# Optimization experiments

Measured on AMD Instinct MI355X. Metric: run time of the kernel, lower is better.

## Reference

```python
import jax, jax.numpy as jnp
import numpy as np

B, S, H, E, I = 2, 1024, 1024, 8, 512
EPS = 1e-8  # torch F.cosine_similarity eps


def setup_inputs() -> dict:
    key = jax.random.key(0)
    ks = jax.random.split(key, 5)
    return {
        "hidden_states": jax.random.normal(ks[0], (B, S, H), dtype=jnp.float32),
        "expert_embeddings": jax.random.normal(ks[1], (E, H), dtype=jnp.float32),
        # torch init is zeros; -0.03 keeps the zero-selection fallback (which NaNs the
        # original's softmax) from ever triggering while preserving ~half-dense routing
        "gate_threshold": jnp.full((E,), -0.03, dtype=jnp.float32),
        "w_gate": jax.random.normal(ks[2], (E, H, I), dtype=jnp.float32) / np.sqrt(H).astype(np.float32),
        "w_up": jax.random.normal(ks[3], (E, H, I), dtype=jnp.float32) / np.sqrt(H).astype(np.float32),
        "w_down": jax.random.normal(ks[4], (E, I, H), dtype=jnp.float32) / np.sqrt(I).astype(np.float32),
    }


def _forward(hidden_states, expert_embeddings, gate_threshold, w_gate, w_up, w_down):
    b, s, h = hidden_states.shape
    n_experts = expert_embeddings.shape[0]
    x = hidden_states.reshape(-1, h)  # [T, H]

    # cosine-similarity routing scores [T, E]
    xn = x / jnp.maximum(jnp.linalg.norm(x, axis=-1, keepdims=True), EPS)
    en = expert_embeddings / jnp.maximum(jnp.linalg.norm(expert_embeddings, axis=-1, keepdims=True), EPS)
    scores = xn @ en.T

    # SiLUHardThreshold forward: hard 0/1 mask (used only as a boolean downstream,
    # so no gradient flows through it in the module's output path)
    routing_mask = (jax.nn.silu(scores - gate_threshold) > 0).astype(scores.dtype)

    # guarantee at least one expert per token: fall back to top-1 score
    num_sel = routing_mask.sum(axis=-1)  # [T]
    top1 = jnp.argmax(scores, axis=-1)   # [T]
    routing_mask_final = jnp.where((num_sel == 0)[:, None],
                                   jax.nn.one_hot(top1, n_experts, dtype=scores.dtype),
                                   routing_mask)

    # softmax over selected experts (pre-fallback mask, as in the original)
    masked_scores = jnp.where(routing_mask > 0, scores, -jnp.inf)
    routing_weights = jax.nn.softmax(masked_scores.astype(jnp.float32), axis=-1).astype(x.dtype)
    gates = routing_weights * routing_mask_final  # [T, E] combine weights

    # per-expert Qwen3 SwiGLU MLP: down(silu(gate(x)) * up(x)); dense over experts,
    # gated combine is the vectorized equivalent of the gather/MLP/index_add loop
    hmid = jax.nn.silu(jnp.einsum('th,ehi->eti', x, w_gate)) * jnp.einsum('th,ehi->eti', x, w_up)  # [E,T,I]
    out = jnp.einsum('eti,eih,te->th', hmid, w_down, gates)  # [T, H]

    return out.reshape(b, s, h), scores


def reference(hidden_states, expert_embeddings, gate_threshold, w_gate, w_up, w_down):
    # returns (final_hidden_states [B,S,H], router_logits [T,E])
    return _forward(hidden_states, expert_embeddings, gate_threshold, w_gate, w_up, w_down)
```

## Files before the change

### kernel.cpp

```cpp
#include <hip/hip_runtime.h>
#include <hip/hip_bf16.h>
#include <stdint.h>

#define T_TOK 2048
#define H_DIM 1024
#define E_NUM 8
#define I_DIM 512
#define KDOWN (E_NUM * I_DIM)
#define EPSR 1e-8f

typedef short s16x8 __attribute__((ext_vector_type(8)));
typedef float f32x4 __attribute__((ext_vector_type(4)));

static __device__ __forceinline__ uint16_t f2bf(float f) {
    union { float f; uint32_t i; } v; v.f = f;
    uint32_t lsb = (v.i >> 16) & 1u;
    v.i += 0x7fffu + lsb;
    return (uint16_t)(v.i >> 16);
}

static __device__ __forceinline__ void gll16(const void* g, void* l) {
    __builtin_amdgcn_global_load_lds(
        (const __attribute__((address_space(1))) void*)g,
        (__attribute__((address_space(3))) void*)l, 16, 0, 0);
}

__global__ __launch_bounds__(256) void prep_kernel(
    const float* __restrict__ wg, const float* __restrict__ wu,
    const float* __restrict__ wd, uint16_t* __restrict__ wB,
    uint16_t* __restrict__ wdT,
    const float* __restrict__ x, const float* __restrict__ emb,
    const float* __restrict__ thr, float* __restrict__ scores_out,
    float* __restrict__ gates, uint16_t* __restrict__ xb) {
    __shared__ union {
        float tile[64][68];
        struct { float semb[E_NUM * H_DIM]; float senorm[E_NUM]; } r;
    } sm;
    const int bid = blockIdx.x;
    const int tid = threadIdx.x;

    if (bid < 3072) {
        const int bz = bid >> 7, by = (bid >> 3) & 15, bx = bid & 7;
        const int g16 = tid >> 4, l16 = (tid & 15) * 4;
        if (bz < 16) {
            const int e = bz & 7;
            const int isU = (bz >= 8);
            const float* src = (isU ? wu : wg) + (long)e * H_DIM * I_DIM;
            const int r0 = by * 64, c0 = bx * 64;
            #pragma unroll
            for (int it = 0; it < 4; ++it) {
                int r = it * 16 + g16;
                *(float4*)&sm.tile[r][l16] = *(const float4*)(src + (long)(r0 + r) * I_DIM + c0 + l16);
            }
            __syncthreads();
            #pragma unroll
            for (int it = 0; it < 4; ++it) {
                int oc = it * 16 + g16;
                int i = c0 + oc;
                ushort4 o;
                o.x = f2bf(sm.tile[l16 + 0][oc]);
                o.y = f2bf(sm.tile[l16 + 1][oc]);
                o.z = f2bf(sm.tile[l16 + 2][oc]);
                o.w = f2bf(sm.tile[l16 + 3][oc]);
                long rbig = ((long)e << 10) + ((i >> 4) << 5) + (isU << 4) + (i & 15);
                *(ushort4*)(wB + rbig * H_DIM + r0 + l16) = o;
            }
        } else {
            const int e = bz - 16;
            const float* src = wd + (long)e * I_DIM * H_DIM;
            uint16_t* dst = wdT + (long)e * I_DIM;
            const int r0 = bx * 64, c0 = by * 64;
            #pragma unroll
            for (int it = 0; it < 4; ++it) {
                int r = it * 16 + g16;
                *(float4*)&sm.tile[r][l16] = *(const float4*)(src + (long)(r0 + r) * H_DIM + c0 + l16);
            }
            __syncthreads();
            #pragma unroll
            for (int it = 0; it < 4; ++it) {
                int oc = it * 16 + g16;
                ushort4 o;
                o.x = f2bf(sm.tile[l16 + 0][oc]);
                o.y = f2bf(sm.tile[l16 + 1][oc]);
                o.z = f2bf(sm.tile[l16 + 2][oc]);
                o.w = f2bf(sm.tile[l16 + 3][oc]);
                *(ushort4*)(dst + (long)(c0 + oc) * KDOWN + r0 + l16) = o;
            }
        }
        return;
    }
    const int rb = bid - 3072;
    const int lane = tid & 63;
    const int wave = tid >> 6;
    for (int i = tid; i < E_NUM * H_DIM; i += 256) sm.r.semb[i] = emb[i];
    __syncthreads();
    for (int e = wave; e < E_NUM; e += 4) {
        float s = 0.f;
        #pragma unroll
        for (int c = 0; c < 16; ++c) { float v = sm.r.semb[e * H_DIM + lane + 64 * c]; s += v * v; }
        #pragma unroll
        for (int off = 32; off; off >>= 1) s += __shfl_xor(s, off);
        if (lane == 0) sm.r.senorm[e] = fmaxf(sqrtf(s), EPSR);
    }
    __syncthreads();
    const int t = rb * 4 + wave;
    const float* xt = x + (long)t * H_DIM;
    uint16_t* xbt = xb + (long)t * H_DIM;
    float nrm = 0.f, dot[E_NUM];
    #pragma unroll
    for (int e = 0; e < E_NUM; ++e) dot[e] = 0.f;
    #pragma unroll
    for (int c = 0; c < 16; ++c) {
        float v = xt[lane + 64 * c];
        xbt[lane + 64 * c] = f2bf(v);
        nrm += v * v;
        #pragma unroll
        for (int e = 0; e < E_NUM; ++e) dot[e] += v * sm.r.semb[e * H_DIM + lane + 64 * c];
    }
    #pragma unroll
    for (int off = 32; off; off >>= 1) {
        nrm += __shfl_xor(nrm, off);
        #pragma unroll
        for (int e = 0; e < E_NUM; ++e) dot[e] += __shfl_xor(dot[e], off);
    }
    float xn = fmaxf(sqrtf(nrm), EPSR);
    float sc[E_NUM], sel[E_NUM];
    float msel = -1e30f, mall = -1e30f;
    int nsel = 0, arg = 0;
    #pragma unroll
    for (int e = 0; e < E_NUM; ++e) {
        sc[e] = dot[e] / (xn * sm.r.senorm[e]);
        float d = sc[e] - thr[e];
        sel[e] = (d > 0.f) ? 1.f : 0.f;
        if (d > 0.f) { nsel++; msel = fmaxf(msel, sc[e]); }
        if (sc[e] > mall) { mall = sc[e]; arg = e; }
    }
    float w[E_NUM], den = 0.f;
    #pragma unroll
    for (int e = 0; e < E_NUM; ++e) { w[e] = (sel[e] > 0.f) ? __expf(sc[e] - msel) : 0.f; den += w[e]; }
    if (lane == 0) {
        #pragma unroll
        for (int e = 0; e < E_NUM; ++e) {
            scores_out[t * E_NUM + e] = sc[e];
            gates[t * E_NUM + e] = (nsel > 0) ? (w[e] / den) : ((e == arg) ? 1.f : 0.f);
        }
    }
}

__global__ __launch_bounds__(512, 2) void moe_gateup_kernel(
    const uint16_t* __restrict__ xb,
    const uint16_t* __restrict__ wB,
    const float* __restrict__ gates,
    uint16_t* __restrict__ hmid) {
    const int bid = blockIdx.x;
    const int xcd = bid & 7, j = bid >> 3;
    const int by = xcd * 4 + (j >> 3);
    const int bx = j & 7;
    const int t0 = bx * 256;
    const int n0 = by * 256;
    const int e  = by >> 2;

    __shared__ uint16_t sA[4][256][32];
    __shared__ uint16_t sB[4][256][32];
    __shared__ float sGate[256];

    const int tid  = threadIdx.x;
    const int lane = tid & 63;
    const int wave = tid >> 6;
    const int wm = wave >> 2, wn = wave & 3;

    if (tid < 256) sGate[tid] = gates[(t0 + tid) * E_NUM + e];
    __syncthreads();

    const int lr = lane >> 2;
    const int cl = ((lane & 3) ^ ((lane >> 3) & 3)) * 8;
    const uint16_t* gA = xb + (long)(t0 + wave * 16 + lr) * H_DIM + cl;
    const uint16_t* gB = wB + (long)(n0 + wave * 16 + lr) * H_DIM + cl;

#define STA(sl, kt) do { \
        gll16(gA + (long)(kt) * 32,                &sA[sl][wave * 16][0]); \
        gll16(gA + 128L * H_DIM + (long)(kt) * 32, &sA[sl][128 + wave * 16][0]); } while (0)
#define STB(sl, kt) do { \
        gll16(gB + (long)(kt) * 32,                &sB[sl][wave * 16][0]); \
        gll16(gB + 128L * H_DIM + (long)(kt) * 32, &sB[sl][128 + wave * 16][0]); } while (0)

    const int q = lane >> 4, r16 = lane & 15;
    const int pc = (q ^ ((r16 >> 1) & 3)) * 8;

    f32x4 acc[8][4] = {};

    STA(0, 0); STB(0, 0);
    STA(1, 1); STB(1, 1);
    STA(2, 2); STB(2, 2);

    #pragma unroll 1
    for (int s = 0; s < 32; ++s) {
        const int sl = s & 3;
        if (s < 30)       asm volatile("s_waitcnt vmcnt(8)" ::: "memory");
        else if (s == 30) asm volatile("s_waitcnt vmcnt(4)" ::: "memory");
        else              asm volatile("s_waitcnt vmcnt(0)" ::: "memory");
        __builtin_amdgcn_s_barrier();
        asm volatile("" ::: "memory");
        if (s + 3 < 32) { STA((s + 3) & 3, s + 3); STB((s + 3) & 3, s + 3); }
        s16x8 af[8], bf[4];
        #pragma unroll
        for (int m = 0; m < 8; ++m)
            af[m] = *(const s16x8*)&sA[sl][wm * 128 + m * 16 + r16][pc];
        #pragma unroll
        for (int n = 0; n < 4; ++n)
            bf[n] = *(const s16x8*)&sB[sl][wn * 64 + n * 16 + r16][pc];
        __builtin_amdgcn_s_setprio(1);
        #pragma unroll
        for (int m = 0; m < 8; ++m)
            #pragma unroll
            for (int n = 0; n < 4; ++n)
                acc[m][n] = __builtin_amdgcn_mfma_f32_16x16x32_bf16(af[m], bf[n], acc[m][n], 0, 0, 0);
        __builtin_amdgcn_s_setprio(0);
    }
#undef STA
#undef STB

    #pragma unroll
    for (int m = 0; m < 8; ++m) {
        #pragma unroll
        for (int rr = 0; rr < 4; ++rr) {
            const int trow = wm * 128 + m * 16 + q * 4 + rr;
            const float gate = sGate[trow];
            const long tglob = t0 + trow;
            #pragma unroll
            for (int p = 0; p < 2; ++p) {
                float g = acc[m][2 * p][rr], u = acc[m][2 * p + 1][rr];
                float h = gate * (g / (1.f + __expf(-g))) * u;
                const int cb = n0 + wn * 64 + p * 32;
                const int i = (((cb & 1023) >> 5) << 4) + r16;
                hmid[tglob * KDOWN + e * I_DIM + i] = f2bf(h);
            }
        }
    }
}

__global__ __launch_bounds__(256, 2) void moe_down_kernel(
    const uint16_t* __restrict__ hmid,
    const uint16_t* __restrict__ wdT,
    float* __restrict__ out,
    float* __restrict__ parts) {
    const int bid = blockIdx.x + 8 * (blockIdx.y + 16 * blockIdx.z);
    const int r  = bid & 7;
    const int j  = bid >> 3;
    const int h0 = ((r & 1) * 4 + (j & 3)) * 128;
    const int t0 = ((r >> 1) * 4 + ((j >> 2) & 3)) * 128;
    const int kz = j >> 4;
    const int kst = kz * 1024;
    __shared__ uint16_t sA[4][128][32];
    __shared__ uint16_t sB[4][128][32];
    const int tid  = threadIdx.x;
    const int lane = tid & 63;
    const int wave = tid >> 6;
    const int wm = wave >> 1, wn = wave & 1;

    const int lr = lane >> 2;
    const int cl = ((lane & 3) ^ ((lane >> 3) & 3)) * 8;
    const uint16_t* gA = hmid + (long)(t0 + wave * 32 + lr) * KDOWN + kst + cl;
    const uint16_t* gB = wdT  + (long)(h0 + wave * 32 + lr) * KDOWN + kst + cl;

#define STA(sl, kt) do { \
        gll16(gA + (long)(kt) * 32,               &sA[sl][wave * 32][0]); \
        gll16(gA + 16L * KDOWN + (long)(kt) * 32, &sA[sl][wave * 32 + 16][0]); } while (0)
#define STB(sl, kt) do { \
        gll16(gB + (long)(kt) * 32,               &sB[sl][wave * 32][0]); \
        gll16(gB + 16L * KDOWN + (long)(kt) * 32, &sB[sl][wave * 32 + 16][0]); } while (0)

    f32x4 acc[4][4] = {};
    const int q = lane >> 4, r16 = lane & 15;
    const int pc = (q ^ ((r16 >> 1) & 3)) * 8;

    STA(0, 0); STB(0, 0);
    STA(1, 1); STB(1, 1);
    STA(2, 2); STB(2, 2);

    #pragma unroll 1
    for (int s = 0; s < 32; ++s) {
        const int sl = s & 3;
        if (s < 30)       asm volatile("s_waitcnt vmcnt(8)" ::: "memory");
        else if (s == 30) asm volatile("s_waitcnt vmcnt(4)" ::: "memory");
        else              asm volatile("s_waitcnt vmcnt(0)" ::: "memory");
        __builtin_amdgcn_s_barrier();
        asm volatile("" ::: "memory");
        if (s + 3 < 32) { STA((s + 3) & 3, s + 3); STB((s + 3) & 3, s + 3); }
        s16x8 af[4], bf[4];
        #pragma unroll
        for (int m = 0; m < 4; ++m)
            af[m] = *(const s16x8*)&sA[sl][wm * 64 + m * 16 + r16][pc];
        #pragma unroll
        for (int n = 0; n < 4; ++n)
            bf[n] = *(const s16x8*)&sB[sl][wn * 64 + n * 16 + r16][pc];
        __builtin_amdgcn_s_setprio(1);
        #pragma unroll
        for (int m = 0; m < 4; ++m)
            #pragma unroll
            for (int n = 0; n < 4; ++n)
                acc[m][n] = __builtin_amdgcn_mfma_f32_16x16x32_bf16(af[m], bf[n], acc[m][n], 0, 0, 0);
        __builtin_amdgcn_s_setprio(0);
    }
#undef STA
#undef STB

    float* dst = (kz == 0) ? out : (parts + (long)(kz - 1) * T_TOK * H_DIM);
    #pragma unroll
    for (int m = 0; m < 4; ++m) {
        #pragma unroll
        for (int rr = 0; rr < 4; ++rr) {
            const int t = t0 + wm * 64 + m * 16 + q * 4 + rr;
            #pragma unroll
            for (int n = 0; n < 4; ++n)
                dst[(long)t * H_DIM + h0 + wn * 64 + n * 16 + r16] = acc[m][n][rr];
        }
    }
}

__global__ __launch_bounds__(256) void reduce_kernel(float* __restrict__ out,
                                                     const float* __restrict__ parts) {
    long i = ((long)blockIdx.x * 256 + threadIdx.x) * 4;
    float4 a = *(const float4*)(out + i);
    #pragma unroll
    for (int j = 0; j < 3; ++j) {
        float4 b = *(const float4*)(parts + (long)j * T_TOK * H_DIM + i);
        a.x += b.x; a.y += b.y; a.z += b.z; a.w += b.w;
    }
    *(float4*)(out + i) = a;
}

extern "C" void kernel_launch(void* const* d_in, const int* in_sizes, int n_in,
                              void* d_out, int out_size, void* d_ws, size_t ws_size,
                              hipStream_t stream) {
    const float* x    = (const float*)d_in[0];
    const float* emb  = (const float*)d_in[1];
    const float* thr  = (const float*)d_in[2];
    const float* wg   = (const float*)d_in[3];
    const float* wu   = (const float*)d_in[4];
    const float* wd   = (const float*)d_in[5];
    float* out    = (float*)d_out;
    float* scores = out + (size_t)T_TOK * H_DIM;

    uint8_t* ws = (uint8_t*)d_ws;
    uint16_t* xb   = (uint16_t*)(ws);
    uint16_t* wB   = (uint16_t*)(ws + (size_t)4  * 1048576);
    uint16_t* wdT  = (uint16_t*)(ws + (size_t)20 * 1048576);
    uint16_t* hmid = (uint16_t*)(ws + (size_t)28 * 1048576);
    float*    gates = (float*)  (ws + (size_t)44 * 1048576);
    float*    parts = (float*)  (ws + (size_t)48 * 1048576);

    prep_kernel<<<3072 + T_TOK / 4, 256, 0, stream>>>(
        wg, wu, wd, wB, wdT, x, emb, thr, scores, gates, xb);
    moe_gateup_kernel<<<256, 512, 0, stream>>>(xb, wB, gates, hmid);
    moe_down_kernel<<<dim3(H_DIM / 128, T_TOK / 128, 4), 256, 0, stream>>>(hmid, wdT, out, parts);
    reduce_kernel<<<(T_TOK * H_DIM) / 1024, 256, 0, stream>>>(out, parts);
}
```

Before: 187.6 us.

## Split GEMM main loops into two ping-pong phases interleaving loads and MFMA

Both GEMM main loops now run each k-step in two halves. Each half loads part of the B fragments, issues one of the A or B global-to-LDS prefetches, and runs half of the MFMAs, with extra barriers placed between the halves. The aim is to interleave memory issue with matrix work across waves and spread out LDS and global traffic. The cost is four barriers per iteration instead of one, and the vmcnt bookkeeping now has to match the new issue order.

```diff
diff --git a/kernel.cpp b/kernel.cpp
--- a/kernel.cpp
+++ b/kernel.cpp
@@ -192,30 +192,51 @@
     STA(0, 0); STB(0, 0);
     STA(1, 1); STB(1, 1);
     STA(2, 2); STB(2, 2);
+    asm volatile("s_waitcnt vmcnt(8)" ::: "memory");
+    __builtin_amdgcn_s_barrier();
+    asm volatile("" ::: "memory");
 
     #pragma unroll 1
     for (int s = 0; s < 32; ++s) {
         const int sl = s & 3;
-        if (s < 30)       asm volatile("s_waitcnt vmcnt(8)" ::: "memory");
-        else if (s == 30) asm volatile("s_waitcnt vmcnt(4)" ::: "memory");
-        else              asm volatile("s_waitcnt vmcnt(0)" ::: "memory");
-        __builtin_amdgcn_s_barrier();
-        asm volatile("" ::: "memory");
-        if (s + 3 < 32) { STA((s + 3) & 3, s + 3); STB((s + 3) & 3, s + 3); }
         s16x8 af[8], bf[4];
         #pragma unroll
         for (int m = 0; m < 8; ++m)
             af[m] = *(const s16x8*)&sA[sl][wm * 128 + m * 16 + r16][pc];
-        #pragma unroll
-        for (int n = 0; n < 4; ++n)
-            bf[n] = *(const s16x8*)&sB[sl][wn * 64 + n * 16 + r16][pc];
+        bf[0] = *(const s16x8*)&sB[sl][wn * 64 + 0 * 16 + r16][pc];
+        bf[1] = *(const s16x8*)&sB[sl][wn * 64 + 1 * 16 + r16][pc];
+        if (s + 3 < 32) STA((s + 3) & 3, s + 3);
+        asm volatile("" ::: "memory");
+        __builtin_amdgcn_s_barrier();
+        asm volatile("" ::: "memory");
         __builtin_amdgcn_s_setprio(1);
         #pragma unroll
-        for (int m = 0; m < 8; ++m)
-            #pragma unroll
-            for (int n = 0; n < 4; ++n)
-                acc[m][n] = __builtin_amdgcn_mfma_f32_16x16x32_bf16(af[m], bf[n], acc[m][n], 0, 0, 0);
+        for (int m = 0; m < 8; ++m) {
+            acc[m][0] = __builtin_amdgcn_mfma_f32_16x16x32_bf16(af[m], bf[0], acc[m][0], 0, 0, 0);
+            acc[m][1] = __builtin_amdgcn_mfma_f32_16x16x32_bf16(af[m], bf[1], acc[m][1], 0, 0, 0);
+        }
         __builtin_amdgcn_s_setprio(0);
+        asm volatile("" ::: "memory");
+        __builtin_amdgcn_s_barrier();
+        asm volatile("" ::: "memory");
+        bf[2] = *(const s16x8*)&sB[sl][wn * 64 + 2 * 16 + r16][pc];
+        bf[3] = *(const s16x8*)&sB[sl][wn * 64 + 3 * 16 + r16][pc];
+        if (s + 3 < 32) STB((s + 3) & 3, s + 3);
+        if (s < 29)      asm volatile("s_waitcnt vmcnt(8)" ::: "memory");
+        else if (s == 29) asm volatile("s_waitcnt vmcnt(4)" ::: "memory");
+        else             asm volatile("s_waitcnt vmcnt(0)" ::: "memory");
+        __builtin_amdgcn_s_barrier();
+        asm volatile("" ::: "memory");
+        __builtin_amdgcn_s_setprio(1);
+        #pragma unroll
+        for (int m = 0; m < 8; ++m) {
+            acc[m][2] = __builtin_amdgcn_mfma_f32_16x16x32_bf16(af[m], bf[2], acc[m][2], 0, 0, 0);
+            acc[m][3] = __builtin_amdgcn_mfma_f32_16x16x32_bf16(af[m], bf[3], acc[m][3], 0, 0, 0);
+        }
+        __builtin_amdgcn_s_setprio(0);
+        asm volatile("" ::: "memory");
+        __builtin_amdgcn_s_barrier();
+        asm volatile("" ::: "memory");
     }
 #undef STA
 #undef STB
@@ -277,30 +298,51 @@
     STA(0, 0); STB(0, 0);
     STA(1, 1); STB(1, 1);
     STA(2, 2); STB(2, 2);
+    asm volatile("s_waitcnt vmcnt(8)" ::: "memory");
+    __builtin_amdgcn_s_barrier();
+    asm volatile("" ::: "memory");
 
     #pragma unroll 1
     for (int s = 0; s < 32; ++s) {
         const int sl = s & 3;
-        if (s < 30)       asm volatile("s_waitcnt vmcnt(8)" ::: "memory");
-        else if (s == 30) asm volatile("s_waitcnt vmcnt(4)" ::: "memory");
-        else              asm volatile("s_waitcnt vmcnt(0)" ::: "memory");
-        __builtin_amdgcn_s_barrier();
-        asm volatile("" ::: "memory");
-        if (s + 3 < 32) { STA((s + 3) & 3, s + 3); STB((s + 3) & 3, s + 3); }
         s16x8 af[4], bf[4];
         #pragma unroll
         for (int m = 0; m < 4; ++m)
             af[m] = *(const s16x8*)&sA[sl][wm * 64 + m * 16 + r16][pc];
-        #pragma unroll
-        for (int n = 0; n < 4; ++n)
-            bf[n] = *(const s16x8*)&sB[sl][wn * 64 + n * 16 + r16][pc];
+        bf[0] = *(const s16x8*)&sB[sl][wn * 64 + 0 * 16 + r16][pc];
+        bf[1] = *(const s16x8*)&sB[sl][wn * 64 + 1 * 16 + r16][pc];
+        if (s + 3 < 32) STA((s + 3) & 3, s + 3);
+        asm volatile("" ::: "memory");
+        __builtin_amdgcn_s_barrier();
+        asm volatile("" ::: "memory");
         __builtin_amdgcn_s_setprio(1);
         #pragma unroll
-        for (int m = 0; m < 4; ++m)
-            #pragma unroll
-            for (int n = 0; n < 4; ++n)
-                acc[m][n] = __builtin_amdgcn_mfma_f32_16x16x32_bf16(af[m], bf[n], acc[m][n], 0, 0, 0);
+        for (int m = 0; m < 4; ++m) {
+            acc[m][0] = __builtin_amdgcn_mfma_f32_16x16x32_bf16(af[m], bf[0], acc[m][0], 0, 0, 0);
+            acc[m][1] = __builtin_amdgcn_mfma_f32_16x16x32_bf16(af[m], bf[1], acc[m][1], 0, 0, 0);
+        }
         __builtin_amdgcn_s_setprio(0);
+        asm volatile("" ::: "memory");
+        __builtin_amdgcn_s_barrier();
+        asm volatile("" ::: "memory");
+        bf[2] = *(const s16x8*)&sB[sl][wn * 64 + 2 * 16 + r16][pc];
+        bf[3] = *(const s16x8*)&sB[sl][wn * 64 + 3 * 16 + r16][pc];
+        if (s + 3 < 32) STB((s + 3) & 3, s + 3);
+        if (s < 29)      asm volatile("s_waitcnt vmcnt(8)" ::: "memory");
+        else if (s == 29) asm volatile("s_waitcnt vmcnt(4)" ::: "memory");
+        else             asm volatile("s_waitcnt vmcnt(0)" ::: "memory");
+        __builtin_amdgcn_s_barrier();
+        asm volatile("" ::: "memory");
+        __builtin_amdgcn_s_setprio(1);
+        #pragma unroll
+        for (int m = 0; m < 4; ++m) {
+            acc[m][2] = __builtin_amdgcn_mfma_f32_16x16x32_bf16(af[m], bf[2], acc[m][2], 0, 0, 0);
+            acc[m][3] = __builtin_amdgcn_mfma_f32_16x16x32_bf16(af[m], bf[3], acc[m][3], 0, 0, 0);
+        }
+        __builtin_amdgcn_s_setprio(0);
+        asm volatile("" ::: "memory");
+        __builtin_amdgcn_s_barrier();
+        asm volatile("" ::: "memory");
     }
 #undef STA
 #undef STB
```

Result: faster. 178.4 us (-4.9%).
